# Kernel optimization log

Measured on AMD Instinct MI355X. Metric: run time of the kernel, lower is better.

## Reference

```python
import jax, jax.numpy as jnp
import numpy as np

B, U, V = 4, 64, 256
IN_DIM, STATE_DIM, CODE_DIM = 768, 768, 384
NUM_HEADS, HEAD_DIM = 8, 64
INNER = NUM_HEADS * HEAD_DIM  # 512
SCALE = HEAD_DIM ** 0.5


def _ln(x, g, b, eps=1e-5):
    mu = jnp.mean(x, axis=-1, keepdims=True)
    var = jnp.var(x, axis=-1, keepdims=True)
    return (x - mu) * jax.lax.rsqrt(var + eps) * g + b


def setup_inputs() -> dict:
    key = jax.random.key(0)
    ks = jax.random.split(key, 12)
    def w(k, shape, s=0.02):
        return jax.random.normal(k, shape, jnp.float32) * s
    return {
        "receiver_states": jax.random.normal(ks[0], (B, U, STATE_DIM), jnp.float32),
        "receiver_codes": jax.random.normal(ks[1], (B, U, CODE_DIM), jnp.float32),
        "sender_states": jax.random.normal(ks[2], (B, V, IN_DIM), jnp.float32),
        "ln_r_g": jnp.ones((STATE_DIM,), jnp.float32),
        "ln_r_b": jnp.zeros((STATE_DIM,), jnp.float32),
        "ln_s_g": jnp.ones((IN_DIM,), jnp.float32),
        "ln_s_b": jnp.zeros((IN_DIM,), jnp.float32),
        "Wq": w(ks[3], (STATE_DIM, INNER)), "bq": jnp.zeros((INNER,), jnp.float32), "Wmq": w(ks[4], (CODE_DIM, STATE_DIM)),
        "Wk": w(ks[5], (IN_DIM, INNER)),   "bk": jnp.zeros((INNER,), jnp.float32), "Wmk": w(ks[6], (CODE_DIM, IN_DIM)),
        "Wv": w(ks[7], (IN_DIM, INNER)),   "bv": jnp.zeros((INNER,), jnp.float32), "Wmv": w(ks[8], (CODE_DIM, IN_DIM)),
        "We": w(ks[9], (INNER, STATE_DIM)), "be": jnp.zeros((STATE_DIM,), jnp.float32), "Wme": w(ks[10], (CODE_DIM, INNER)),
        "gamma": jnp.ones((STATE_DIM,), jnp.float32),  # LayerScale, init 1.0
    }


def reference(receiver_states, receiver_codes, sender_states,
              ln_r_g, ln_r_b, ln_s_g, ln_s_b,
              Wq, bq, Wmq, Wk, bk, Wmk, Wv, bv, Wmv, We, be, Wme, gamma):
    r = _ln(receiver_states, ln_r_g, ln_r_b)   # (b,u,ds)
    s = _ln(sender_states, ln_s_g, ln_s_b)     # (b,v,di)
    # ModFC: y = (x * (1 + ctx @ Wm)) @ W + b  (code-conditioned input modulation)
    q = (r * (1.0 + receiver_codes @ Wmq)) @ Wq + bq          # (b,u,inner)
    mk = 1.0 + receiver_codes @ Wmk                           # (b,u,di)
    mv = 1.0 + receiver_codes @ Wmv                           # (b,u,di)
    xs = s[:, :, None, :]                                     # (b,v,1,di)
    k = (xs * mk[:, None, :, :]) @ Wk + bk                    # (b,v,u,inner)
    v = (xs * mv[:, None, :, :]) @ Wv + bv                    # (b,v,u,inner)
    qh = q.reshape(B, U, NUM_HEADS, HEAD_DIM)
    kh = k.reshape(B, V, U, NUM_HEADS, HEAD_DIM)
    vh = v.reshape(B, V, U, NUM_HEADS, HEAD_DIM)
    scores = jnp.einsum('buhc,bvuhc->bhuv', qh, kh) / SCALE   # (b,h,u,v)
    weights = jax.nn.softmax(scores, axis=-1)
    msg = jnp.einsum('bhuv,bvuhc->buhc', weights, vh).reshape(B, U, INNER)
    out = (msg * (1.0 + receiver_codes @ Wme)) @ We + be      # exit ModFC -> (b,u,ds)
    out = out * gamma                                         # LayerScale
    return receiver_states + out                              # residual
```

## Files before the change

### kernel.cpp

```cpp
#include <hip/hip_runtime.h>


#define DD 768
#define CDIM 384
#define NH 8
#define HD 64
#define INNER 512
#define VV 256

__device__ __forceinline__ float4 ldf4(const float* p) {
  return *(const float4*)(p);
}

__device__ __forceinline__ void fma4(float4& a, float s, const float4& b) {
  a.x += s * b.x; a.y += s * b.y; a.z += s * b.z; a.w += s * b.w;
}

__device__ __forceinline__ void fma_chunk8(const float* __restrict__ Aw,
                                           int lda, int kk, const float4* b,
                                           float4* acc) {
#pragma unroll
  for (int rg = 0; rg < 4; rg++) {
    const float* ap = Aw + (rg * 2) * lda + kk;
    float4 a0l = ldf4(ap);
    float4 a0h = ldf4(ap + 4);
    float4 a1l = ldf4(ap + lda);
    float4 a1h = ldf4(ap + lda + 4);
    float4* ac = acc + rg * 2;
    fma4(ac[0], a0l.x, b[0]); fma4(ac[1], a1l.x, b[0]);
    fma4(ac[0], a0l.y, b[1]); fma4(ac[1], a1l.y, b[1]);
    fma4(ac[0], a0l.z, b[2]); fma4(ac[1], a1l.z, b[2]);
    fma4(ac[0], a0l.w, b[3]); fma4(ac[1], a1l.w, b[3]);
    fma4(ac[0], a0h.x, b[4]); fma4(ac[1], a1h.x, b[4]);
    fma4(ac[0], a0h.y, b[5]); fma4(ac[1], a1h.y, b[5]);
    fma4(ac[0], a0h.z, b[6]); fma4(ac[1], a1h.z, b[6]);
    fma4(ac[0], a0h.w, b[7]); fma4(ac[1], a1h.w, b[7]);
  }
}

template <int KQ, int NS>
__device__ __forceinline__ void gcore8(const float* __restrict__ Aw, int lda,
                                       const float* __restrict__ Bp,
                                       float4* acc) {
  float4 b0[8], b1[8];
  const float* Bq = Bp;
#pragma unroll
  for (int i = 0; i < 8; i++) b0[i] = ldf4(Bq + (size_t)i * NS);
  Bq += (size_t)8 * NS;
#pragma unroll 1
  for (int kk = 0; kk + 16 <= KQ; kk += 16) {
#pragma unroll
    for (int i = 0; i < 8; i++) b1[i] = ldf4(Bq + (size_t)i * NS);
    Bq += (size_t)8 * NS;
    fma_chunk8(Aw, lda, kk, b0, acc);
    if (kk + 16 < KQ) {
#pragma unroll
      for (int i = 0; i < 8; i++) b0[i] = ldf4(Bq + (size_t)i * NS);
      Bq += (size_t)8 * NS;
    }
    fma_chunk8(Aw, lda, kk + 8, b1, acc);
  }
}

__device__ __forceinline__ void kred(float4* acc, float* RED, int wid,
                                     int kl) {
  __syncthreads();
  float4* R4 = (float4*)RED;
  int rg = wid & 1, kh = wid >> 1;
  if (kh) {
#pragma unroll
    for (int r = 0; r < 8; r++) R4[(rg * 8 + r) * 64 + kl] = acc[r];
  }
  __syncthreads();
  if (!kh) {
#pragma unroll
    for (int r = 0; r < 8; r++) {
      float4 v = R4[(rg * 8 + r) * 64 + kl];
      acc[r].x += v.x; acc[r].y += v.y; acc[r].z += v.z; acc[r].w += v.w;
    }
  }
}

__global__ __launch_bounds__(256, 2) void k_s1(
    const float* __restrict__ ss, const float* __restrict__ rs,
    const float* __restrict__ g_s, const float* __restrict__ b_s,
    const float* __restrict__ g_r, const float* __restrict__ b_r,
    const float* __restrict__ codes, const float* __restrict__ Wmq,
    const float* __restrict__ Wmk, const float* __restrict__ Wmv,
    const float* __restrict__ Wme, const float* __restrict__ Wk,
    float* __restrict__ s_ln, float* __restrict__ r_ln,
    float* __restrict__ cp, float* __restrict__ WkT) {
  __shared__ __align__(16) float SB[6144];
  int bid = blockIdx.x, t = threadIdx.x;
  if (bid < 176) {
    int nc = bid % 11, mb = bid / 11;
    int base = nc * 256;
    const float* W; int N, colW;
    if (base < 768)       { W = Wmq; N = DD;    colW = base; }
    else if (base < 1536) { W = Wmk; N = DD;    colW = base - 768; }
    else if (base < 2304) { W = Wmv; N = DD;    colW = base - 1536; }
    else                  { W = Wme; N = INNER; colW = base - 2304; }
    int m0 = mb * 16;
#pragma unroll
    for (int p = 0; p < 24; p++) {
      int idx = p * 256 + t, r = idx / 384, k = idx % 384;
      SB[idx] = codes[(size_t)(m0 + r) * CDIM + k];
    }
    __syncthreads();
    int kl = t & 63, wid = t >> 6, rg = wid & 1, kh = wid >> 1;
    float4 acc[8] = {};
    const float* Aw = SB + (rg * 8) * 384 + kh * 192;
    if (N == DD)
      gcore8<192, DD>(Aw, 384, W + (size_t)(kh * 192) * DD + colW + 4 * kl, acc);
    else
      gcore8<192, INNER>(Aw, 384, W + (size_t)(kh * 192) * INNER + colW + 4 * kl, acc);
    kred(acc, SB, wid, kl);
    if (!kh) {
      int gcol = base + 4 * kl;
#pragma unroll
      for (int j = 0; j < 8; j++)
        *(float4*)(cp + (size_t)(m0 + rg * 8 + j) * 2816 + gcol) = acc[j];
    }
  } else if (bid < 272) {
    int tid = bid - 176;
    int d0 = (tid >> 3) * 64, c0 = (tid & 7) * 64;
    int j = t & 63, i0 = t >> 6;
#pragma unroll
    for (int p = 0; p < 16; p++) {
      int i = p * 4 + i0;
      SB[i * 65 + j] = Wk[(size_t)(d0 + i) * INNER + c0 + j];
    }
    __syncthreads();
#pragma unroll
    for (int p = 0; p < 16; p++) {
      int i = p * 4 + i0;
      WkT[(size_t)(c0 + i) * DD + d0 + j] = SB[j * 65 + i];
    }
  } else {
    int rr = (bid - 272) * 4 + (t >> 6);
    const float *x, *g, *bb; float* y; int r;
    if (rr < 1024) { x = ss; g = g_s; bb = b_s; y = s_ln; r = rr; }
    else           { x = rs; g = g_r; bb = b_r; y = r_ln; r = rr - 1024; }
    const float* xr = x + (size_t)r * DD;
    int lane = t & 63;
    float v[12];
    float s = 0.f, sq = 0.f;
#pragma unroll
    for (int j = 0; j < 12; j++) {
      v[j] = xr[lane + 64 * j];
      s += v[j]; sq += v[j] * v[j];
    }
    for (int o = 32; o > 0; o >>= 1) {
      s += __shfl_down(s, o, 64); sq += __shfl_down(sq, o, 64);
    }
    s = __shfl(s, 0, 64); sq = __shfl(sq, 0, 64);
    float mu = s * (1.0f / 768.0f);
    float var = sq * (1.0f / 768.0f) - mu * mu;
    float rstd = rsqrtf(var + 1e-5f);
    float* yr = y + (size_t)r * DD;
#pragma unroll
    for (int j = 0; j < 12; j++) {
      int d = lane + 64 * j;
      yr[d] = (v[j] - mu) * rstd * g[d] + bb[d];
    }
  }
}

__global__ __launch_bounds__(256, 2) void k_s2(
    const float* __restrict__ s_ln, const float* __restrict__ r_ln,
    const float* __restrict__ cp, const float* __restrict__ Wq,
    float* __restrict__ sT, float* __restrict__ qp) {
  __shared__ __align__(16) float SB[4160];
  int bid = blockIdx.x, t = threadIdx.x;
  if (bid < 128) {
    int ks = bid & 3, tile = bid >> 2, nc = tile & 1, mb = tile >> 1;
    int m0 = mb * 16, col0 = nc * 256, k0 = ks * 192;
#pragma unroll
    for (int p = 0; p < 12; p++) {
      int idx = p * 256 + t, r = idx / 192, k = idx % 192;
      int d = k0 + k;
      float mqv = cp[(size_t)(m0 + r) * 2816 + d] + 1.0f;
      SB[idx] = r_ln[(size_t)(m0 + r) * DD + d] * mqv;
    }
    __syncthreads();
    int kl = t & 63, wid = t >> 6, rg = wid & 1, kh = wid >> 1;
    int col = col0 + 4 * kl;
    float4 acc[8] = {};
    gcore8<96, INNER>(SB + (rg * 8) * 192 + kh * 96, 192,
                      Wq + (size_t)(k0 + kh * 96) * INNER + col, acc);
    kred(acc, SB, wid, kl);
    if (!kh) {
      float* dst = qp + (size_t)ks * (256 * INNER);
#pragma unroll
      for (int j = 0; j < 8; j++)
        *(float4*)(dst + (size_t)(m0 + rg * 8 + j) * INNER + col) = acc[j];
    }
  } else {
    int tid = bid - 128;
    int vt = tid & 3, dt = (tid >> 2) % 12, b = tid / 48;
    int v0 = vt * 64, d0 = dt * 64;
    int j = t & 63, i0 = t >> 6;
#pragma unroll
    for (int p = 0; p < 16; p++) {
      int i = p * 4 + i0;
      SB[i * 65 + j] = s_ln[(size_t)(b * VV + v0 + i) * DD + d0 + j];
    }
    __syncthreads();
#pragma unroll
    for (int p = 0; p < 16; p++) {
      int i = p * 4 + i0;
      sT[((size_t)b * DD + d0 + i) * VV + v0 + j] = SB[j * 65 + i];
    }
  }
}

__global__ __launch_bounds__(256, 2) void k_s3(
    const float* __restrict__ qp, const float* __restrict__ bq,
    const float* __restrict__ WkT, const float* __restrict__ cp,
    const float* __restrict__ bk, float* __restrict__ qm,
    float* __restrict__ qbk) {
  __shared__ __align__(16) float SB[4096];
  int bid = blockIdx.x, t = threadIdx.x;
  int h = bid & 7, dc = (bid >> 3) % 3, mb = bid / 24;
  int m0 = mb * 16;
  {
    int r = t >> 4, c4 = (t & 15) * 4;
    int i = h * HD + c4;
    size_t off = (size_t)(m0 + r) * INNER + i;
    float4 q0 = ldf4(qp + off), q1 = ldf4(qp + 131072 + off);
    float4 q2 = ldf4(qp + 262144 + off), q3 = ldf4(qp + 393216 + off);
    float4 bq4 = ldf4(bq + i);
    float4 s;
    s.x = q0.x + q1.x + q2.x + q3.x + bq4.x;
    s.y = q0.y + q1.y + q2.y + q3.y + bq4.y;
    s.z = q0.z + q1.z + q2.z + q3.z + bq4.z;
    s.w = q0.w + q1.w + q2.w + q3.w + bq4.w;
    ((float4*)SB)[t] = s;
  }
  __syncthreads();
  if (dc == 0) {
    int m = t >> 4, cg = t & 15;
    const float* bkh = bk + h * HD;
    float p = 0.f;
#pragma unroll
    for (int c = 4 * cg; c < 4 * cg + 4; c++) p += SB[m * HD + c] * bkh[c];
    SB[1024 + t] = p;
  }
  __syncthreads();
  if (dc == 0 && t < 16) {
    float a = 0.f;
#pragma unroll
    for (int i = 0; i < 16; i++) a += SB[1024 + t * 16 + i];
    qbk[(m0 + t) * NH + h] = a;
  }
  int kl = t & 63, wid = t >> 6, rg = wid & 1, kh = wid >> 1;
  int col = dc * 256 + 4 * kl;
  float4 acc[8] = {};
  gcore8<32, DD>(SB + (rg * 8) * HD + kh * 32, HD,
                 WkT + (size_t)(h * HD + kh * 32) * DD + col, acc);
  kred(acc, SB, wid, kl);
  if (!kh) {
#pragma unroll
    for (int j = 0; j < 8; j++) {
      int m = m0 + rg * 8 + j;
      const float* mkp = cp + (size_t)m * 2816 + 768 + col;
      float4 o = {acc[j].x * (mkp[0] + 1.0f), acc[j].y * (mkp[1] + 1.0f),
                  acc[j].z * (mkp[2] + 1.0f), acc[j].w * (mkp[3] + 1.0f)};
      *(float4*)(qm + ((size_t)m * NH + h) * DD + col) = o;
    }
  }
}

__global__ __launch_bounds__(256, 2) void k_s4(
    const float* __restrict__ qm, const float* __restrict__ sT,
    float* __restrict__ scp) {
  __shared__ __align__(16) float SB[4096];
  int bid = blockIdx.x, t = threadIdx.x;
  int ks = bid & 3, b = (bid >> 2) & 3, mb = bid >> 4;
  int gi0 = b * 512 + mb * 16, k0 = ks * 192;
#pragma unroll
  for (int p = 0; p < 12; p++) {
    int idx = p * 256 + t, r = idx / 192, k = idx % 192;
    SB[idx] = qm[(size_t)(gi0 + r) * DD + k0 + k];
  }
  __syncthreads();
  int kl = t & 63, wid = t >> 6, rg = wid & 1, kh = wid >> 1;
  int col = 4 * kl;
  float4 acc[8] = {};
  gcore8<96, VV>(SB + (rg * 8) * 192 + kh * 96, 192,
                 sT + ((size_t)b * DD + k0 + kh * 96) * VV + col, acc);
  kred(acc, SB, wid, kl);
  if (!kh) {
    float* dst = scp + (size_t)ks * (2048 * VV);
#pragma unroll
    for (int j = 0; j < 8; j++)
      *(float4*)(dst + (size_t)(gi0 + rg * 8 + j) * VV + col) = acc[j];
  }
}

__global__ __launch_bounds__(256, 2) void k_s5(
    const float* __restrict__ scp, const float* __restrict__ qbk,
    const float* __restrict__ s_ln, const float* __restrict__ cp,
    float* __restrict__ wsm) {
  __shared__ __align__(16) float SC[4096];
  int bid = blockIdx.x, t = threadIdx.x;
  int dc = bid % 3, up = (bid / 3) % 32, b = bid / 96;
  int gi0 = b * 512 + up * 16;
  float4* SC4 = (float4*)SC;
#pragma unroll
  for (int p = 0; p < 4; p++) {
    int idx4 = p * 256 + t;
    int r = idx4 >> 6, c4 = (idx4 & 63) * 4;
    size_t o = (size_t)(gi0 + r) * VV + c4;
    float4 v0 = ldf4(scp + o), v1 = ldf4(scp + 524288 + o);
    float4 v2 = ldf4(scp + 1048576 + o), v3 = ldf4(scp + 1572864 + o);
    int m = b * 64 + up * 2 + (r >> 3), h = r & 7;
    float qb = qbk[m * NH + h];
    float4 s;
    s.x = (v0.x + v1.x + v2.x + v3.x + qb) * 0.125f;
    s.y = (v0.y + v1.y + v2.y + v3.y + qb) * 0.125f;
    s.z = (v0.z + v1.z + v2.z + v3.z + qb) * 0.125f;
    s.w = (v0.w + v1.w + v2.w + v3.w + qb) * 0.125f;
    SC4[idx4] = s;
  }
  __syncthreads();
  int wid = t >> 6, lane = t & 63;
#pragma unroll
  for (int j = 0; j < 4; j++) {
    int r = wid * 4 + j;
    float x0 = SC[r * 256 + lane],       x1 = SC[r * 256 + lane + 64];
    float x2 = SC[r * 256 + lane + 128], x3 = SC[r * 256 + lane + 192];
    float mx = fmaxf(fmaxf(x0, x1), fmaxf(x2, x3));
    for (int o = 1; o < 64; o <<= 1) mx = fmaxf(mx, __shfl_xor(mx, o, 64));
    float e0 = __expf(x0 - mx), e1 = __expf(x1 - mx);
    float e2 = __expf(x2 - mx), e3 = __expf(x3 - mx);
    float sm = e0 + e1 + e2 + e3;
    for (int o = 1; o < 64; o <<= 1) sm += __shfl_xor(sm, o, 64);
    float rinv = 1.0f / sm;
    SC[r * 256 + lane] = e0 * rinv;       SC[r * 256 + lane + 64] = e1 * rinv;
    SC[r * 256 + lane + 128] = e2 * rinv; SC[r * 256 + lane + 192] = e3 * rinv;
  }
  __syncthreads();
  int kl = t & 63, rg = wid & 1, kh = wid >> 1;
  int col = dc * 256 + 4 * kl;
  float4 acc[8] = {};
  gcore8<128, DD>(SC + (rg * 8) * 256 + kh * 128, 256,
                  s_ln + (size_t)(b * VV + kh * 128) * DD + col, acc);
  kred(acc, SC, wid, kl);
  if (!kh) {
#pragma unroll
    for (int j = 0; j < 8; j++) {
      int m = b * 64 + up * 2 + rg;
      const float* mvp = cp + (size_t)m * 2816 + 1536 + col;
      float4 o = {acc[j].x * (mvp[0] + 1.0f), acc[j].y * (mvp[1] + 1.0f),
                  acc[j].z * (mvp[2] + 1.0f), acc[j].w * (mvp[3] + 1.0f)};
      *(float4*)(wsm + ((size_t)j * 256 + m) * DD + col) = o;
    }
  }
}

__global__ __launch_bounds__(256, 2) void k_s6(
    const float* __restrict__ wsm, const float* __restrict__ Wv,
    float* __restrict__ mmp) {
  __shared__ __align__(16) float AL[6144];
  int bid = blockIdx.x, t = threadIdx.x;
  int hp = bid & 1, ks = (bid >> 1) & 7, mb = bid >> 4;
  int h0 = hp * 4, m0 = mb * 16, k0 = ks * 96;
#pragma unroll
  for (int p = 0; p < 24; p++) {
    int idx = p * 256 + t;
    int e = idx / 1536, rem = idx % 1536, r = rem / 96, k = rem % 96;
    AL[idx] = wsm[((size_t)(h0 + e) * 256 + m0 + r) * DD + k0 + k];
  }
  __syncthreads();
  int kl = t & 63, wid = t >> 6, rg = wid & 1, kh = wid >> 1;
  int hs = kl >> 4, c4 = 4 * (kl & 15);
  int colg = h0 * HD + hs * HD + c4;
  const float* Aw = AL + hs * 1536 + (rg * 8) * 96 + kh * 48;
  float4 acc[8] = {};
  gcore8<48, INNER>(Aw, 96, Wv + (size_t)(k0 + kh * 48) * INNER + colg, acc);
  kred(acc, AL, wid, kl);
  if (!kh) {
    float* dst = mmp + (size_t)ks * (256 * INNER);
#pragma unroll
    for (int j = 0; j < 8; j++)
      *(float4*)(dst + (size_t)(m0 + rg * 8 + j) * INNER + colg) = acc[j];
  }
}

__global__ __launch_bounds__(256, 2) void k_s7(
    const float* __restrict__ mmp, const float* __restrict__ bvv,
    const float* __restrict__ cp, const float* __restrict__ We,
    float* __restrict__ op) {
  __shared__ __align__(16) float AL[4096];
  int bid = blockIdx.x, t = threadIdx.x;
  int ks = bid & 7, dc = (bid >> 3) % 3, mb = bid / 24;
  int m0 = mb * 16, k0 = ks * 64;
  {
    int r = t >> 4, k4 = (t & 15) * 4;
    int i = k0 + k4;
    size_t off = (size_t)(m0 + r) * INNER + i;
    float4 v = ldf4(mmp + off);
    float4 m1 = ldf4(mmp + 131072 + off), m2 = ldf4(mmp + 262144 + off);
    float4 m3 = ldf4(mmp + 393216 + off), m4 = ldf4(mmp + 524288 + off);
    float4 m5 = ldf4(mmp + 655360 + off), m6 = ldf4(mmp + 786432 + off);
    float4 m7 = ldf4(mmp + 917504 + off);
    v.x = v.x + m1.x + m2.x + m3.x + m4.x + m5.x + m6.x + m7.x;
    v.y = v.y + m1.y + m2.y + m3.y + m4.y + m5.y + m6.y + m7.y;
    v.z = v.z + m1.z + m2.z + m3.z + m4.z + m5.z + m6.z + m7.z;
    v.w = v.w + m1.w + m2.w + m3.w + m4.w + m5.w + m6.w + m7.w;
    float4 me = ldf4(cp + (size_t)(m0 + r) * 2816 + 2304 + i);
    float4 bv4 = ldf4(bvv + i);
    float4 res = {(v.x + bv4.x) * (me.x + 1.0f), (v.y + bv4.y) * (me.y + 1.0f),
                  (v.z + bv4.z) * (me.z + 1.0f), (v.w + bv4.w) * (me.w + 1.0f)};
    ((float4*)AL)[t] = res;
  }
  __syncthreads();
  int kl = t & 63, wid = t >> 6, rg = wid & 1, kh = wid >> 1;
  int col = dc * 256 + 4 * kl;
  float4 acc[8] = {};
  gcore8<32, DD>(AL + (rg * 8) * 64 + kh * 32, 64,
                 We + (size_t)(k0 + kh * 32) * DD + col, acc);
  kred(acc, AL, wid, kl);
  if (!kh) {
    float* dst = op + (size_t)ks * (256 * DD);
#pragma unroll
    for (int j = 0; j < 8; j++)
      *(float4*)(dst + (size_t)(m0 + rg * 8 + j) * DD + col) = acc[j];
  }
}

__global__ __launch_bounds__(256, 2) void k_s8(
    const float* __restrict__ op, const float* __restrict__ be,
    const float* __restrict__ gamma, const float* __restrict__ rs,
    float* __restrict__ outp) {
  int m = blockIdx.x, t = threadIdx.x;
  if (t < 192) {
    int d = 4 * t;
    size_t off = (size_t)m * DD + d;
    float4 v = ldf4(op + off);
    float4 o1 = ldf4(op + 196608 + off), o2 = ldf4(op + 393216 + off);
    float4 o3 = ldf4(op + 589824 + off), o4 = ldf4(op + 786432 + off);
    float4 o5 = ldf4(op + 983040 + off), o6 = ldf4(op + 1179648 + off);
    float4 o7 = ldf4(op + 1376256 + off);
    v.x = v.x + o1.x + o2.x + o3.x + o4.x + o5.x + o6.x + o7.x;
    v.y = v.y + o1.y + o2.y + o3.y + o4.y + o5.y + o6.y + o7.y;
    v.z = v.z + o1.z + o2.z + o3.z + o4.z + o5.z + o6.z + o7.z;
    v.w = v.w + o1.w + o2.w + o3.w + o4.w + o5.w + o6.w + o7.w;
    float4 bev = ldf4(be + d), gv = ldf4(gamma + d);
    float4 rv = ldf4(rs + off);
    float4 out = {rv.x + (v.x + bev.x) * gv.x, rv.y + (v.y + bev.y) * gv.y,
                  rv.z + (v.z + bev.z) * gv.z, rv.w + (v.w + bev.w) * gv.w};
    *(float4*)(outp + off) = out;
  }
}

extern "C" void kernel_launch(void* const* d_in, const int* in_sizes, int n_in,
                              void* d_out, int out_size, void* d_ws, size_t ws_size,
                              hipStream_t stream) {
  const float* rs     = (const float*)d_in[0];
  const float* codes  = (const float*)d_in[1];
  const float* ss     = (const float*)d_in[2];
  const float* ln_r_g = (const float*)d_in[3];
  const float* ln_r_b = (const float*)d_in[4];
  const float* ln_s_g = (const float*)d_in[5];
  const float* ln_s_b = (const float*)d_in[6];
  const float* Wq  = (const float*)d_in[7];
  const float* bq  = (const float*)d_in[8];
  const float* Wk  = (const float*)d_in[10];
  const float* bk  = (const float*)d_in[11];
  const float* Wmq = (const float*)d_in[9];
  const float* Wmk = (const float*)d_in[12];
  const float* Wv  = (const float*)d_in[13];
  const float* bv  = (const float*)d_in[14];
  const float* Wmv = (const float*)d_in[15];
  const float* We  = (const float*)d_in[16];
  const float* be  = (const float*)d_in[17];
  const float* Wme = (const float*)d_in[18];
  const float* gamma = (const float*)d_in[19];

  float* w = (float*)d_ws;
  float* s_ln = w;
  float* r_ln = w + 786432;
  float* WkT  = w + 983040;
  float* qp   = w + 1376256;
  float* sT   = w + 1900544;
  float* cp   = w + 2686976;
  float* qbk  = w + 3407872;
  float* qm   = w + 3409920;
  float* scp  = w + 4982784;
  float* wsm  = qm;
  float* mmp  = r_ln;
  float* op   = scp;

  k_s1<<<dim3(592), 256, 0, stream>>>(ss, rs, ln_s_g, ln_s_b, ln_r_g, ln_r_b,
                                      codes, Wmq, Wmk, Wmv, Wme, Wk,
                                      s_ln, r_ln, cp, WkT);
  k_s2<<<dim3(320), 256, 0, stream>>>(s_ln, r_ln, cp, Wq, sT, qp);
  k_s3<<<dim3(384), 256, 0, stream>>>(qp, bq, WkT, cp, bk, qm, qbk);
  k_s4<<<dim3(512), 256, 0, stream>>>(qm, sT, scp);
  k_s5<<<dim3(384), 256, 0, stream>>>(scp, qbk, s_ln, cp, wsm);
  k_s6<<<dim3(256), 256, 0, stream>>>(wsm, Wv, mmp);
  k_s7<<<dim3(384), 256, 0, stream>>>(mmp, bv, cp, We, op);
  k_s8<<<dim3(256), 256, 0, stream>>>(op, be, gamma, rs, (float*)d_out);
}
```

Measured before the change: 183.1 us.

## Fuse query-key projection and score GEMM into one kernel via shared memory

Merges the kernel that projects queries through Wk with the score GEMM against transposed sender states. The modulated qm tile now stays in shared memory instead of making a round trip through global memory, and one launch is removed. The K dimension is split into three 256-wide chunks instead of four 192-wide ones, so the softmax kernel sums three partials. Each block now runs two GEMMs in sequence, and the grid has fewer blocks than the old score kernel.

```diff
diff --git a/kernel.cpp b/kernel.cpp
--- a/kernel.cpp
+++ b/kernel.cpp
@@ -214,15 +214,15 @@
   }
 }
 
-__global__ __launch_bounds__(256, 2) void k_s3(
+__global__ __launch_bounds__(256, 2) void k_s34(
     const float* __restrict__ qp, const float* __restrict__ bq,
     const float* __restrict__ WkT, const float* __restrict__ cp,
-    const float* __restrict__ bk, float* __restrict__ qm,
-    float* __restrict__ qbk) {
+    const float* __restrict__ bk, const float* __restrict__ sT,
+    float* __restrict__ scp, float* __restrict__ qbk) {
   __shared__ __align__(16) float SB[4096];
   int bid = blockIdx.x, t = threadIdx.x;
-  int h = bid & 7, dc = (bid >> 3) % 3, mb = bid / 24;
-  int m0 = mb * 16;
+  int mb = bid & 15, h = (bid >> 4) & 7, ks = bid >> 7;
+  int m0 = mb * 16, b = mb >> 2, k0 = ks * 256;
   {
     int r = t >> 4, c4 = (t & 15) * 4;
     int i = h * HD + c4;
@@ -238,7 +238,7 @@
     ((float4*)SB)[t] = s;
   }
   __syncthreads();
-  if (dc == 0) {
+  if (ks == 0) {
     int m = t >> 4, cg = t & 15;
     const float* bkh = bk + h * HD;
     float p = 0.f;
@@ -247,54 +247,40 @@
     SB[1024 + t] = p;
   }
   __syncthreads();
-  if (dc == 0 && t < 16) {
+  if (ks == 0 && t < 16) {
     float a = 0.f;
 #pragma unroll
     for (int i = 0; i < 16; i++) a += SB[1024 + t * 16 + i];
     qbk[(m0 + t) * NH + h] = a;
   }
   int kl = t & 63, wid = t >> 6, rg = wid & 1, kh = wid >> 1;
-  int col = dc * 256 + 4 * kl;
   float4 acc[8] = {};
   gcore8<32, DD>(SB + (rg * 8) * HD + kh * 32, HD,
-                 WkT + (size_t)(h * HD + kh * 32) * DD + col, acc);
+                 WkT + (size_t)(h * HD + kh * 32) * DD + k0 + 4 * kl, acc);
   kred(acc, SB, wid, kl);
+  __syncthreads();
   if (!kh) {
 #pragma unroll
     for (int j = 0; j < 8; j++) {
       int m = m0 + rg * 8 + j;
-      const float* mkp = cp + (size_t)m * 2816 + 768 + col;
+      const float* mkp = cp + (size_t)m * 2816 + 768 + k0 + 4 * kl;
       float4 o = {acc[j].x * (mkp[0] + 1.0f), acc[j].y * (mkp[1] + 1.0f),
                   acc[j].z * (mkp[2] + 1.0f), acc[j].w * (mkp[3] + 1.0f)};
-      *(float4*)(qm + ((size_t)m * NH + h) * DD + col) = o;
-    }
-  }
-}
-
-__global__ __launch_bounds__(256, 2) void k_s4(
-    const float* __restrict__ qm, const float* __restrict__ sT,
-    float* __restrict__ scp) {
-  __shared__ __align__(16) float SB[4096];
-  int bid = blockIdx.x, t = threadIdx.x;
-  int ks = bid & 3, b = (bid >> 2) & 3, mb = bid >> 4;
-  int gi0 = b * 512 + mb * 16, k0 = ks * 192;
-#pragma unroll
-  for (int p = 0; p < 12; p++) {
-    int idx = p * 256 + t, r = idx / 192, k = idx % 192;
-    SB[idx] = qm[(size_t)(gi0 + r) * DD + k0 + k];
-  }
-  __syncthreads();
-  int kl = t & 63, wid = t >> 6, rg = wid & 1, kh = wid >> 1;
-  int col = 4 * kl;
-  float4 acc[8] = {};
-  gcore8<96, VV>(SB + (rg * 8) * 192 + kh * 96, 192,
-                 sT + ((size_t)b * DD + k0 + kh * 96) * VV + col, acc);
-  kred(acc, SB, wid, kl);
+      *(float4*)(SB + (rg * 8 + j) * 256 + 4 * kl) = o;
+    }
+  }
+  __syncthreads();
+  float4 acc2[8] = {};
+  gcore8<128, VV>(SB + (rg * 8) * 256 + kh * 128, 256,
+                  sT + ((size_t)b * DD + k0 + kh * 128) * VV + 4 * kl, acc2);
+  kred(acc2, SB, wid, kl);
   if (!kh) {
     float* dst = scp + (size_t)ks * (2048 * VV);
 #pragma unroll
-    for (int j = 0; j < 8; j++)
-      *(float4*)(dst + (size_t)(gi0 + rg * 8 + j) * VV + col) = acc[j];
+    for (int j = 0; j < 8; j++) {
+      int gi = (m0 + rg * 8 + j) * NH + h;
+      *(float4*)(dst + (size_t)gi * VV + 4 * kl) = acc2[j];
+    }
   }
 }
 
@@ -313,14 +299,14 @@
     int r = idx4 >> 6, c4 = (idx4 & 63) * 4;
     size_t o = (size_t)(gi0 + r) * VV + c4;
     float4 v0 = ldf4(scp + o), v1 = ldf4(scp + 524288 + o);
-    float4 v2 = ldf4(scp + 1048576 + o), v3 = ldf4(scp + 1572864 + o);
+    float4 v2 = ldf4(scp + 1048576 + o);
     int m = b * 64 + up * 2 + (r >> 3), h = r & 7;
     float qb = qbk[m * NH + h];
     float4 s;
-    s.x = (v0.x + v1.x + v2.x + v3.x + qb) * 0.125f;
-    s.y = (v0.y + v1.y + v2.y + v3.y + qb) * 0.125f;
-    s.z = (v0.z + v1.z + v2.z + v3.z + qb) * 0.125f;
-    s.w = (v0.w + v1.w + v2.w + v3.w + qb) * 0.125f;
+    s.x = (v0.x + v1.x + v2.x + qb) * 0.125f;
+    s.y = (v0.y + v1.y + v2.y + qb) * 0.125f;
+    s.z = (v0.z + v1.z + v2.z + qb) * 0.125f;
+    s.w = (v0.w + v1.w + v2.w + qb) * 0.125f;
     SC4[idx4] = s;
   }
   __syncthreads();
@@ -497,8 +483,7 @@
                                       codes, Wmq, Wmk, Wmv, Wme, Wk,
                                       s_ln, r_ln, cp, WkT);
   k_s2<<<dim3(320), 256, 0, stream>>>(s_ln, r_ln, cp, Wq, sT, qp);
-  k_s3<<<dim3(384), 256, 0, stream>>>(qp, bq, WkT, cp, bk, qm, qbk);
-  k_s4<<<dim3(512), 256, 0, stream>>>(qm, sT, scp);
+  k_s34<<<dim3(384), 256, 0, stream>>>(qp, bq, WkT, cp, bk, sT, scp, qbk);
   k_s5<<<dim3(384), 256, 0, stream>>>(scp, qbk, s_ln, cp, wsm);
   k_s6<<<dim3(256), 256, 0, stream>>>(wsm, Wv, mmp);
   k_s7<<<dim3(384), 256, 0, stream>>>(mmp, bv, cp, We, op);
```

Result: no change. 179.9 us, median of 2 (-1.8%).
